# Performance work log

Hardware: AMD Instinct MI355X
Metric: run time of the kernel (lower is better)

The kernel has to match this reference:

```python
import jax, jax.numpy as jnp
import numpy as np

BS, SL, D, H = 8, 1024, 1024, 16
DK = D // H


def setup_inputs() -> dict:
    key = jax.random.key(0)
    ks = jax.random.split(key, 12)
    mk = lambda k, shape, s=1.0: jax.random.normal(k, shape, dtype=jnp.float32) * s
    return {
        "q": mk(ks[0], (BS, SL, D)),
        "k": mk(ks[1], (BS, SL, D)),
        "v": mk(ks[2], (BS, SL, D)),
        "mask": jax.random.randint(ks[3], (BS, SL), 0, 2, dtype=jnp.int32),
        "wq": mk(ks[4], (D, D), 0.02), "bq": jnp.zeros((D,), jnp.float32),
        "wk": mk(ks[5], (D, D), 0.02), "bk": jnp.zeros((D,), jnp.float32),
        "wv": mk(ks[6], (D, D), 0.02), "bv": jnp.zeros((D,), jnp.float32),
        "wo": mk(ks[7], (D, D), 0.02), "bo": jnp.zeros((D,), jnp.float32),
    }


def reference(q, k, v, mask, wq, bq, wk, bk, wv, bv, wo, bo):
    bs, sl, d = q.shape
    # linear projections (torch Linear: x @ W^T + b), split heads -> [b, h, s, dk]
    def proj(x, w, b):
        return (x @ w.T + b).reshape(bs, sl, H, DK).transpose(0, 2, 1, 3)
    qh, kh, vh = proj(q, wq, bq), proj(k, wk, bk), proj(v, wv, bv)
    # scaled scores [b, h, sq, sk]
    scores = jnp.einsum("bhqd,bhkd->bhqk", qh, kh) / jnp.sqrt(jnp.float32(DK))
    # mask query rows: mask [b, s] -> [b, 1, s, 1]
    m = mask[:, None, :, None]
    scores = jnp.where(m == 0, jnp.float32(-1e9), scores)
    # NOTE: original code computes transform(scores) but discards it; the output
    # path uses the raw masked/scaled scores (dropout is identity at eval).
    ctx = jnp.einsum("bhqk,bhkd->bhqd", scores, vh)  # [b, h, s, dk]
    concat = ctx.transpose(0, 2, 1, 3).reshape(bs, sl, d)
    return concat @ wo.T + bo
```

## Files before the change

### kernel.cpp

```cpp
#include <hip/hip_runtime.h>
#include <hip/hip_bf16.h>
#include <stdint.h>

#define BSZ 8
#define SLEN 1024
#define DMODEL 1024
#define NH 16
#define HD 64
#define MROWS (BSZ * SLEN)

typedef __bf16 bf16_t;
typedef __bf16 bf16x8 __attribute__((ext_vector_type(8)));
typedef __bf16 bf16x4 __attribute__((ext_vector_type(4)));
typedef float f32x4 __attribute__((ext_vector_type(4)));

__device__ __forceinline__ void gload_lds16(const void* g, void* l) {
    __builtin_amdgcn_global_load_lds(
        (const __attribute__((address_space(1))) unsigned int*)g,
        (__attribute__((address_space(3))) unsigned int*)l,
        16, 0, 0);
}

__global__ __launch_bounds__(256) void cvt_f32_to_bf16(
    const float* __restrict__ src, bf16_t* __restrict__ dst, int n4) {
    int i = blockIdx.x * blockDim.x + threadIdx.x;
    if (i >= n4) return;
    const float4 v = reinterpret_cast<const float4*>(src)[i];
    bf16x4 o;
    o[0] = (bf16_t)v.x; o[1] = (bf16_t)v.y; o[2] = (bf16_t)v.z; o[3] = (bf16_t)v.w;
    reinterpret_cast<bf16x4*>(dst)[i] = o;
}

template <int FINAL>
__global__ __launch_bounds__(256) void gemm_bt(
    const bf16_t* __restrict__ A, const bf16_t* __restrict__ B,
    void* __restrict__ C, const float* __restrict__ bias,
    const float* __restrict__ trow, const int* __restrict__ mask,
    int M, int N, int K, int bstride) {
    __shared__ bf16_t As[128 * 32];
    __shared__ bf16_t Bs[128 * 32];
    const int tid = threadIdx.x;
    const int m0 = blockIdx.y * 128;
    const int n0 = blockIdx.x * 128;
    const bf16_t* Bp = B + (size_t)(m0 >> 10) * (size_t)bstride;

    const int srow = tid >> 2;
    const int scol = (tid & 3) * 8;
    const bf16_t* Ag = A + (size_t)(m0 + srow) * K + scol;
    const bf16_t* Bg = Bp + (size_t)(n0 + srow) * K + scol;
    bf16_t* Asl = As + srow * 32 + scol;
    bf16_t* Bsl = Bs + srow * 32 + scol;

    const int lane = tid & 63;
    const int wave = tid >> 6;
    const int wr = (wave >> 1) * 64;
    const int wc = (wave & 1) * 64;
    const int lr = lane & 15;
    const int lk = (lane >> 4) * 8;

    f32x4 acc[4][4] = {};

    for (int kt = 0; kt < K; kt += 32) {
        gload_lds16(Ag + kt, Asl);
        gload_lds16(Ag + kt + (size_t)64 * K, Asl + 64 * 32);
        gload_lds16(Bg + kt, Bsl);
        gload_lds16(Bg + kt + (size_t)64 * K, Bsl + 64 * 32);
        __syncthreads();
        bf16x8 aw[4], bw[4];
#pragma unroll
        for (int i = 0; i < 4; ++i)
            aw[i] = *reinterpret_cast<const bf16x8*>(&As[(wr + i * 16 + lr) * 32 + lk]);
#pragma unroll
        for (int i = 0; i < 4; ++i)
            bw[i] = *reinterpret_cast<const bf16x8*>(&Bs[(wc + i * 16 + lr) * 32 + lk]);
#pragma unroll
        for (int mi = 0; mi < 4; ++mi)
#pragma unroll
            for (int ni = 0; ni < 4; ++ni)
                acc[mi][ni] = __builtin_amdgcn_mfma_f32_16x16x32_bf16(
                    aw[mi], bw[ni], acc[mi][ni], 0, 0, 0);
        __syncthreads();
    }

    const int lq4 = (lane >> 4) * 4;
    if (FINAL == 0) {
        bf16_t* Co = (bf16_t*)C;
#pragma unroll
        for (int mi = 0; mi < 4; ++mi)
#pragma unroll
            for (int ni = 0; ni < 4; ++ni) {
                const int col = n0 + wc + ni * 16 + lr;
                const float bcol = bias[col];
#pragma unroll
                for (int r = 0; r < 4; ++r) {
                    const int row = m0 + wr + mi * 16 + lq4 + r;
                    Co[(size_t)row * N + col] = (bf16_t)(acc[mi][ni][r] + bcol);
                }
            }
    } else {
        float* Co = (float*)C;
#pragma unroll
        for (int mi = 0; mi < 4; ++mi)
#pragma unroll
            for (int ni = 0; ni < 4; ++ni) {
                const int col = n0 + wc + ni * 16 + lr;
                const float bcol = bias[col];
#pragma unroll
                for (int r = 0; r < 4; ++r) {
                    const int row = m0 + wr + mi * 16 + lq4 + r;
                    const int b = row >> 10, s = row & 1023;
                    float v;
                    if (mask[b * SLEN + s]) v = acc[mi][ni][r] * 0.125f + bcol;
                    else v = trow[(size_t)b * DMODEL + col];
                    Co[(size_t)row * N + col] = v;
                }
            }
    }
}

__global__ __launch_bounds__(512) void compute_w(
    const bf16_t* __restrict__ Kh, const bf16_t* __restrict__ Vh,
    float* __restrict__ Wpart) {
    __shared__ float Ksf[64 * 64];
    __shared__ float Vsf[64 * 64];
    const int h = blockIdx.x;
    const int b = blockIdx.y;
    const int ks = blockIdx.z;
    const int tid = threadIdx.x;
    const int dd = tid & 63;
    const int eg = tid >> 6;
    const int srow = tid >> 3;
    const int sseg = (tid & 7) * 8;

    float acc[8] = {};
    for (int kc = 0; kc < 8; ++kc) {
        const int kbase = ks * 512 + kc * 64;
        const size_t roff = (size_t)(b * SLEN + kbase + srow) * DMODEL + h * HD + sseg;
        bf16x8 kv = *reinterpret_cast<const bf16x8*>(&Kh[roff]);
        bf16x8 vv = *reinterpret_cast<const bf16x8*>(&Vh[roff]);
#pragma unroll
        for (int j = 0; j < 8; ++j) {
            Ksf[srow * 64 + sseg + j] = (float)kv[j];
            Vsf[srow * 64 + sseg + j] = (float)vv[j];
        }
        __syncthreads();
#pragma unroll 4
        for (int kk = 0; kk < 64; ++kk) {
            const float vval = Vsf[kk * 64 + dd];
#pragma unroll
            for (int i = 0; i < 8; ++i)
                acc[i] += Ksf[kk * 64 + eg * 8 + i] * vval;
        }
        __syncthreads();
    }
    float* Wo = Wpart + (((size_t)ks * BSZ + b) * NH + h) * 4096;
#pragma unroll
    for (int i = 0; i < 8; ++i)
        Wo[(eg * 8 + i) * 64 + dd] = acc[i];
}

__global__ __launch_bounds__(256) void colsum_v(
    const bf16_t* __restrict__ Vh, float* __restrict__ Spart) {
    const int dseg = blockIdx.x;
    const int b = blockIdx.y;
    const int ks = blockIdx.z;
    const int d = dseg * 256 + threadIdx.x;
    float acc = 0.f;
#pragma unroll 8
    for (int k = ks * 128; k < ks * 128 + 128; ++k)
        acc += (float)Vh[(size_t)(b * SLEN + k) * DMODEL + d];
    Spart[((size_t)ks * BSZ + b) * DMODEL + d] = acc;
}

__global__ __launch_bounds__(256) void compute_t(
    const float* __restrict__ Spart, const float* __restrict__ wo,
    const float* __restrict__ bo, float* __restrict__ t) {
    __shared__ float Ss[DMODEL];
    const int b = blockIdx.x >> 8;
    const int j0 = (blockIdx.x & 255) * 4;
    const int tid = threadIdx.x;
#pragma unroll
    for (int i = 0; i < 4; ++i) {
        const int d = i * 256 + tid;
        float s = 0.f;
#pragma unroll
        for (int ks = 0; ks < 8; ++ks) s += Spart[((size_t)ks * BSZ + b) * DMODEL + d];
        Ss[d] = s;
    }
    __syncthreads();
    const int wave = tid >> 6, lane = tid & 63;
    const int j = j0 + wave;
    f32x4 acc = {};
#pragma unroll
    for (int it = 0; it < 4; ++it) {
        const int idx = it * 256 + lane * 4;
        const f32x4 wv = *reinterpret_cast<const f32x4*>(&wo[(size_t)j * DMODEL + idx]);
        const f32x4 sv = *reinterpret_cast<const f32x4*>(&Ss[idx]);
        acc += wv * sv;
    }
    float tot = acc[0] + acc[1] + acc[2] + acc[3];
#pragma unroll
    for (int off = 1; off < 64; off <<= 1) tot += __shfl_xor(tot, off, 64);
    if (lane == 0) t[(size_t)b * DMODEL + j] = -1e9f * tot + bo[j];
}

__global__ __launch_bounds__(256) void compute_pt(
    const float* __restrict__ Wpart, const float* __restrict__ wo,
    bf16_t* __restrict__ PT) {
    __shared__ float Ws[64 * 65];
    __shared__ float Wos[128 * 64];
    const int jt = blockIdx.x;
    const int h = blockIdx.y;
    const int b = blockIdx.z;
    const int tid = threadIdx.x;
    const int j0 = jt * 128;
    const float* W0 = Wpart + (((size_t)0 * BSZ + b) * NH + h) * 4096;
    const float* W1 = Wpart + (((size_t)1 * BSZ + b) * NH + h) * 4096;
#pragma unroll
    for (int i = 0; i < 16; ++i) {
        const int idx = i * 256 + tid;
        Ws[(idx >> 6) * 65 + (idx & 63)] = W0[idx] + W1[idx];
    }
#pragma unroll
    for (int i = 0; i < 32; ++i) {
        const int idx = i * 256 + tid;
        Wos[idx] = wo[(size_t)(j0 + (idx >> 6)) * DMODEL + h * HD + (idx & 63)];
    }
    __syncthreads();
    const int e = tid & 63;
    const int jb = tid >> 6;
    for (int jj2 = 0; jj2 < 32; ++jj2) {
        const int jj = jb * 32 + jj2;
        float acc = 0.f;
#pragma unroll
        for (int dd = 0; dd < 64; ++dd)
            acc += Wos[jj * 64 + dd] * Ws[e * 65 + dd];
        PT[((size_t)b * SLEN + j0 + jj) * DMODEL + h * HD + e] = (bf16_t)acc;
    }
}

extern "C" void kernel_launch(void* const* d_in, const int* in_sizes, int n_in,
                              void* d_out, int out_size, void* d_ws, size_t ws_size,
                              hipStream_t stream) {
    const float* q  = (const float*)d_in[0];
    const float* k  = (const float*)d_in[1];
    const float* v  = (const float*)d_in[2];
    const int* mask = (const int*)d_in[3];
    const float* wq = (const float*)d_in[4];
    const float* bq = (const float*)d_in[5];
    const float* wk = (const float*)d_in[6];
    const float* bk = (const float*)d_in[7];
    const float* wv = (const float*)d_in[8];
    const float* bv = (const float*)d_in[9];
    const float* wo = (const float*)d_in[10];
    const float* bo = (const float*)d_in[11];

    char* ws = (char*)d_ws;
    const size_t SZ_ACT = (size_t)MROWS * DMODEL * 2;
    const size_t SZ_W = (size_t)DMODEL * DMODEL * 2;
    bf16_t* buf0 = (bf16_t*)(ws);
    bf16_t* buf1 = (bf16_t*)(ws + SZ_ACT);
    bf16_t* buf2 = (bf16_t*)(ws + 2 * SZ_ACT);
    bf16_t* Qh   = (bf16_t*)(ws + 3 * SZ_ACT);
    bf16_t* wqb  = (bf16_t*)(ws + 4 * SZ_ACT);
    bf16_t* wkb  = (bf16_t*)(ws + 4 * SZ_ACT + SZ_W);
    bf16_t* wvb  = (bf16_t*)(ws + 4 * SZ_ACT + 2 * SZ_W);
    float* Wpart = (float*)(ws + 4 * SZ_ACT + 3 * SZ_W);
    float* Spart = (float*)((char*)Wpart + (size_t)2 * 8 * 16 * 4096 * 4);
    float* trow  = (float*)((char*)Spart + (size_t)8 * 8 * 1024 * 4);

    const int n4a = MROWS * DMODEL / 4;
    const int n4w = DMODEL * DMODEL / 4;
    cvt_f32_to_bf16<<<dim3(n4a / 256), 256, 0, stream>>>(q, buf0, n4a);
    cvt_f32_to_bf16<<<dim3(n4a / 256), 256, 0, stream>>>(k, buf1, n4a);
    cvt_f32_to_bf16<<<dim3(n4a / 256), 256, 0, stream>>>(v, buf2, n4a);
    cvt_f32_to_bf16<<<dim3(n4w / 256), 256, 0, stream>>>(wq, wqb, n4w);
    cvt_f32_to_bf16<<<dim3(n4w / 256), 256, 0, stream>>>(wk, wkb, n4w);
    cvt_f32_to_bf16<<<dim3(n4w / 256), 256, 0, stream>>>(wv, wvb, n4w);

    const dim3 gg(DMODEL / 128, MROWS / 128);
    gemm_bt<0><<<gg, 256, 0, stream>>>(buf0, wqb, Qh,   bq, nullptr, nullptr, MROWS, DMODEL, DMODEL, 0);
    gemm_bt<0><<<gg, 256, 0, stream>>>(buf1, wkb, buf0, bk, nullptr, nullptr, MROWS, DMODEL, DMODEL, 0);
    gemm_bt<0><<<gg, 256, 0, stream>>>(buf2, wvb, buf1, bv, nullptr, nullptr, MROWS, DMODEL, DMODEL, 0);

    compute_w<<<dim3(NH, BSZ, 2), 512, 0, stream>>>(buf0, buf1, Wpart);
    colsum_v<<<dim3(4, BSZ, 8), 256, 0, stream>>>(buf1, Spart);
    compute_t<<<dim3(2048), 256, 0, stream>>>(Spart, wo, bo, trow);
    compute_pt<<<dim3(8, NH, BSZ), 256, 0, stream>>>(Wpart, wo, buf2);

    gemm_bt<1><<<gg, 256, 0, stream>>>(Qh, buf2, d_out, bo, trow, mask,
                                       MROWS, DMODEL, DMODEL, SLEN * DMODEL);
}
```

Before: 384.2 us.

## Replace 128x128 GEMM with double-buffered 256x256 swizzled-LDS kernel and batch launches

Replaces the 128x128 single-buffered bf16 GEMM with a 256x256-tile, 512-thread kernel. It double-buffers LDS, prefetches the next K slice with direct global-to-LDS loads while issuing MFMAs, uses an XOR-style swizzle to cut LDS bank conflicts, and raises wave priority around MFMA bursts. The QKV projections are batched into one launch over blockIdx.z when workspace allows, and the six conversion kernels are merged into two. The aim is more data reuse per tile, hidden load latency and less launch overhead. The cost is larger LDS use, which limits occupancy, and a bigger workspace footprint on the roomy path.

```diff
diff --git a/kernel.cpp b/kernel.cpp
--- a/kernel.cpp
+++ b/kernel.cpp
@@ -8,6 +8,7 @@
 #define NH 16
 #define HD 64
 #define MROWS (BSZ * SLEN)
+#define NT 16
 
 typedef __bf16 bf16_t;
 typedef __bf16 bf16x8 __attribute__((ext_vector_type(8)));
@@ -17,102 +18,168 @@
 __device__ __forceinline__ void gload_lds16(const void* g, void* l) {
     __builtin_amdgcn_global_load_lds(
         (const __attribute__((address_space(1))) unsigned int*)g,
-        (__attribute__((address_space(3))) unsigned int*)l,
-        16, 0, 0);
-}
-
-__global__ __launch_bounds__(256) void cvt_f32_to_bf16(
-    const float* __restrict__ src, bf16_t* __restrict__ dst, int n4) {
+        (__attribute__((address_space(3))) unsigned int*)l, 16, 0, 0);
+}
+
+__global__ __launch_bounds__(256) void cvt3(
+    const float* __restrict__ s0, const float* __restrict__ s1, const float* __restrict__ s2,
+    bf16_t* __restrict__ o0, bf16_t* __restrict__ o1, bf16_t* __restrict__ o2, int n4) {
+    const float* s = s0; bf16_t* d = o0;
+    if (blockIdx.y == 1) { s = s1; d = o1; }
+    else if (blockIdx.y == 2) { s = s2; d = o2; }
     int i = blockIdx.x * blockDim.x + threadIdx.x;
     if (i >= n4) return;
-    const float4 v = reinterpret_cast<const float4*>(src)[i];
+    const float4 v = reinterpret_cast<const float4*>(s)[i];
     bf16x4 o;
     o[0] = (bf16_t)v.x; o[1] = (bf16_t)v.y; o[2] = (bf16_t)v.z; o[3] = (bf16_t)v.w;
-    reinterpret_cast<bf16x4*>(dst)[i] = o;
+    reinterpret_cast<bf16x4*>(d)[i] = o;
+}
+
+__device__ __forceinline__ void mfma_quad(f32x4 (&acc)[8][4], int mb,
+                                          const bf16x8 (&afr)[4], const bf16x8 (&bfr)[4]) {
+    __builtin_amdgcn_s_setprio(1);
+#pragma unroll
+    for (int m = 0; m < 4; ++m)
+#pragma unroll
+        for (int n = 0; n < 4; ++n)
+            acc[mb + m][n] = __builtin_amdgcn_mfma_f32_16x16x32_bf16(
+                afr[m], bfr[n], acc[mb + m][n], 0, 0, 0);
+    __builtin_amdgcn_s_setprio(0);
 }
 
 template <int FINAL>
-__global__ __launch_bounds__(256) void gemm_bt(
-    const bf16_t* __restrict__ A, const bf16_t* __restrict__ B,
-    void* __restrict__ C, const float* __restrict__ bias,
-    const float* __restrict__ trow, const int* __restrict__ mask,
-    int M, int N, int K, int bstride) {
-    __shared__ bf16_t As[128 * 32];
-    __shared__ bf16_t Bs[128 * 32];
+__global__ __launch_bounds__(512, 2) void gemm256(
+    const bf16_t* __restrict__ A0, const bf16_t* __restrict__ B0p, void* __restrict__ C0, const float* __restrict__ bias0,
+    const bf16_t* __restrict__ A1, const bf16_t* __restrict__ B1p, void* __restrict__ C1, const float* __restrict__ bias1,
+    const bf16_t* __restrict__ A2, const bf16_t* __restrict__ B2p, void* __restrict__ C2, const float* __restrict__ bias2,
+    const float* __restrict__ trow, const int* __restrict__ mask) {
+    __shared__ __align__(16) bf16_t As[4][256 * 32];
+    __shared__ __align__(16) bf16_t Bs[4][256 * 32];
     const int tid = threadIdx.x;
-    const int m0 = blockIdx.y * 128;
-    const int n0 = blockIdx.x * 128;
-    const bf16_t* Bp = B + (size_t)(m0 >> 10) * (size_t)bstride;
-
-    const int srow = tid >> 2;
-    const int scol = (tid & 3) * 8;
-    const bf16_t* Ag = A + (size_t)(m0 + srow) * K + scol;
-    const bf16_t* Bg = Bp + (size_t)(n0 + srow) * K + scol;
-    bf16_t* Asl = As + srow * 32 + scol;
-    bf16_t* Bsl = Bs + srow * 32 + scol;
-
-    const int lane = tid & 63;
-    const int wave = tid >> 6;
-    const int wr = (wave >> 1) * 64;
-    const int wc = (wave & 1) * 64;
-    const int lr = lane & 15;
-    const int lk = (lane >> 4) * 8;
-
-    f32x4 acc[4][4] = {};
-
-    for (int kt = 0; kt < K; kt += 32) {
-        gload_lds16(Ag + kt, Asl);
-        gload_lds16(Ag + kt + (size_t)64 * K, Asl + 64 * 32);
-        gload_lds16(Bg + kt, Bsl);
-        gload_lds16(Bg + kt + (size_t)64 * K, Bsl + 64 * 32);
-        __syncthreads();
-        bf16x8 aw[4], bw[4];
-#pragma unroll
-        for (int i = 0; i < 4; ++i)
-            aw[i] = *reinterpret_cast<const bf16x8*>(&As[(wr + i * 16 + lr) * 32 + lk]);
-#pragma unroll
-        for (int i = 0; i < 4; ++i)
-            bw[i] = *reinterpret_cast<const bf16x8*>(&Bs[(wc + i * 16 + lr) * 32 + lk]);
-#pragma unroll
-        for (int mi = 0; mi < 4; ++mi)
-#pragma unroll
-            for (int ni = 0; ni < 4; ++ni)
-                acc[mi][ni] = __builtin_amdgcn_mfma_f32_16x16x32_bf16(
-                    aw[mi], bw[ni], acc[mi][ni], 0, 0, 0);
-        __syncthreads();
-    }
-
-    const int lq4 = (lane >> 4) * 4;
+    const int lane = tid & 63, wave = tid >> 6;
+    const int wm = wave >> 2, wn = wave & 3;
+    const int lr = lane & 15, g = lane >> 4;
+
+    const bf16_t* A = A0; const bf16_t* B = B0p; void* C = C0; const float* bias = bias0;
+    if (blockIdx.z == 1) { A = A1; B = B1p; C = C1; bias = bias1; }
+    else if (blockIdx.z == 2) { A = A2; B = B2p; C = C2; bias = bias2; }
+
+    const int m0 = blockIdx.y * 256;
+    const int n0 = blockIdx.x * 256;
+    if (FINAL) B += (size_t)(m0 >> 10) * SLEN * DMODEL;
+
+    const int q0 = wave * 64 + lane, q1 = 512 + q0;
+    const int row0 = q0 >> 2, row1 = q1 >> 2;
+    const int gl0 = ((q0 & 3) - (row0 >> 1)) & 3;
+    const int gl1 = ((q1 & 3) - (row1 >> 1)) & 3;
+    const int sOfs0 = row0 * DMODEL + gl0 * 8;
+    const int sOfs1 = row1 * DMODEL + gl1 * 8;
+    const bf16_t* Ag = A + (size_t)m0 * DMODEL;
+    const bf16_t* Bg = B + (size_t)n0 * DMODEL;
+    char* const AsB = (char*)&As[0][0];
+    char* const BsB = (char*)&Bs[0][0];
+    const int d0 = q0 * 16, d1 = q1 * 16;
+
+    int aoff[8], boff[4];
+#pragma unroll
+    for (int mi = 0; mi < 8; ++mi) {
+        const int r = wm * 128 + mi * 16 + lr;
+        aoff[mi] = r * 64 + (((g + (r >> 1)) & 3) << 4);
+    }
+#pragma unroll
+    for (int ni = 0; ni < 4; ++ni) {
+        const int r = wn * 64 + ni * 16 + lr;
+        boff[ni] = r * 64 + (((g + (r >> 1)) & 3) << 4);
+    }
+
+    f32x4 acc[8][4] = {};
+
+    gload_lds16(Ag + sOfs0, AsB + d0);
+    gload_lds16(Ag + sOfs1, AsB + d1);
+    gload_lds16(Bg + sOfs0, BsB + d0);
+    gload_lds16(Bg + sOfs1, BsB + d1);
+    gload_lds16(Ag + sOfs0 + 32, AsB + 16384 + d0);
+    gload_lds16(Ag + sOfs1 + 32, AsB + 16384 + d1);
+    gload_lds16(Bg + sOfs0 + 32, BsB + 16384 + d0);
+    gload_lds16(Bg + sOfs1 + 32, BsB + 16384 + d1);
+
+    for (int t = 0; t < NT; ++t) {
+        const int cur = t & 1, nxt = cur ^ 1;
+        const int kn = ((t + 1 < NT) ? (t + 1) : 0) * 64;
+        const char* Ac0 = AsB + cur * 32768;
+        const char* Ac1 = Ac0 + 16384;
+        const char* Bc0 = BsB + cur * 32768;
+        const char* Bc1 = Bc0 + 16384;
+        char* An0 = AsB + nxt * 32768; char* An1 = An0 + 16384;
+        char* Bn0 = BsB + nxt * 32768; char* Bn1 = Bn0 + 16384;
+        bf16x8 afr[4], bfr[4];
+
+        asm volatile("s_waitcnt vmcnt(4)" ::: "memory");
+        __builtin_amdgcn_s_barrier();
+        __builtin_amdgcn_sched_barrier(0);
+        gload_lds16(Ag + sOfs0 + kn, An0 + d0);
+        gload_lds16(Ag + sOfs1 + kn, An0 + d1);
+#pragma unroll
+        for (int i = 0; i < 4; ++i) bfr[i] = *reinterpret_cast<const bf16x8*>(Bc0 + boff[i]);
+#pragma unroll
+        for (int i = 0; i < 4; ++i) afr[i] = *reinterpret_cast<const bf16x8*>(Ac0 + aoff[i]);
+        mfma_quad(acc, 0, afr, bfr);
+
+        gload_lds16(Bg + sOfs0 + kn, Bn0 + d0);
+        gload_lds16(Bg + sOfs1 + kn, Bn0 + d1);
+#pragma unroll
+        for (int i = 0; i < 4; ++i) afr[i] = *reinterpret_cast<const bf16x8*>(Ac0 + aoff[4 + i]);
+        mfma_quad(acc, 4, afr, bfr);
+
+        asm volatile("s_waitcnt vmcnt(4)" ::: "memory");
+        __builtin_amdgcn_s_barrier();
+        __builtin_amdgcn_sched_barrier(0);
+        gload_lds16(Ag + sOfs0 + kn + 32, An1 + d0);
+        gload_lds16(Ag + sOfs1 + kn + 32, An1 + d1);
+#pragma unroll
+        for (int i = 0; i < 4; ++i) bfr[i] = *reinterpret_cast<const bf16x8*>(Bc1 + boff[i]);
+#pragma unroll
+        for (int i = 0; i < 4; ++i) afr[i] = *reinterpret_cast<const bf16x8*>(Ac1 + aoff[i]);
+        mfma_quad(acc, 0, afr, bfr);
+
+        gload_lds16(Bg + sOfs0 + kn + 32, Bn1 + d0);
+        gload_lds16(Bg + sOfs1 + kn + 32, Bn1 + d1);
+#pragma unroll
+        for (int i = 0; i < 4; ++i) afr[i] = *reinterpret_cast<const bf16x8*>(Ac1 + aoff[4 + i]);
+        mfma_quad(acc, 4, afr, bfr);
+    }
+
+    const int lq4 = g * 4;
     if (FINAL == 0) {
         bf16_t* Co = (bf16_t*)C;
 #pragma unroll
-        for (int mi = 0; mi < 4; ++mi)
+        for (int mi = 0; mi < 8; ++mi)
 #pragma unroll
             for (int ni = 0; ni < 4; ++ni) {
-                const int col = n0 + wc + ni * 16 + lr;
+                const int col = n0 + wn * 64 + ni * 16 + lr;
                 const float bcol = bias[col];
 #pragma unroll
                 for (int r = 0; r < 4; ++r) {
-                    const int row = m0 + wr + mi * 16 + lq4 + r;
-                    Co[(size_t)row * N + col] = (bf16_t)(acc[mi][ni][r] + bcol);
+                    const int row = m0 + wm * 128 + mi * 16 + lq4 + r;
+                    Co[(size_t)row * DMODEL + col] = (bf16_t)(acc[mi][ni][r] + bcol);
                 }
             }
     } else {
         float* Co = (float*)C;
 #pragma unroll
-        for (int mi = 0; mi < 4; ++mi)
+        for (int mi = 0; mi < 8; ++mi)
 #pragma unroll
             for (int ni = 0; ni < 4; ++ni) {
-                const int col = n0 + wc + ni * 16 + lr;
+                const int col = n0 + wn * 64 + ni * 16 + lr;
                 const float bcol = bias[col];
 #pragma unroll
                 for (int r = 0; r < 4; ++r) {
-                    const int row = m0 + wr + mi * 16 + lq4 + r;
+                    const int row = m0 + wm * 128 + mi * 16 + lq4 + r;
                     const int b = row >> 10, s = row & 1023;
                     float v;
                     if (mask[b * SLEN + s]) v = acc[mi][ni][r] * 0.125f + bcol;
                     else v = trow[(size_t)b * DMODEL + col];
-                    Co[(size_t)row * N + col] = v;
+                    Co[(size_t)row * DMODEL + col] = v;
                 }
             }
     }
@@ -258,36 +325,56 @@
     char* ws = (char*)d_ws;
     const size_t SZ_ACT = (size_t)MROWS * DMODEL * 2;
     const size_t SZ_W = (size_t)DMODEL * DMODEL * 2;
-    bf16_t* buf0 = (bf16_t*)(ws);
-    bf16_t* buf1 = (bf16_t*)(ws + SZ_ACT);
-    bf16_t* buf2 = (bf16_t*)(ws + 2 * SZ_ACT);
-    bf16_t* Qh   = (bf16_t*)(ws + 3 * SZ_ACT);
-    bf16_t* wqb  = (bf16_t*)(ws + 4 * SZ_ACT);
-    bf16_t* wkb  = (bf16_t*)(ws + 4 * SZ_ACT + SZ_W);
-    bf16_t* wvb  = (bf16_t*)(ws + 4 * SZ_ACT + 2 * SZ_W);
-    float* Wpart = (float*)(ws + 4 * SZ_ACT + 3 * SZ_W);
-    float* Spart = (float*)((char*)Wpart + (size_t)2 * 8 * 16 * 4096 * 4);
-    float* trow  = (float*)((char*)Spart + (size_t)8 * 8 * 1024 * 4);
+    const size_t SZ_WPART = (size_t)2 * 8 * 16 * 4096 * 4;
+    const size_t SZ_SPART = (size_t)8 * 8 * 1024 * 4;
+    const size_t SZ_TROW = (size_t)8 * 1024 * 4;
+    const size_t need_roomy = 6 * SZ_ACT + 3 * SZ_W + SZ_WPART + SZ_SPART + SZ_TROW;
+    const bool roomy = ws_size >= need_roomy;
+
+    bf16_t* qb = (bf16_t*)(ws);
+    bf16_t* kb = (bf16_t*)(ws + SZ_ACT);
+    bf16_t* vb = (bf16_t*)(ws + 2 * SZ_ACT);
+    bf16_t* Qh = (bf16_t*)(ws + 3 * SZ_ACT);
+    bf16_t *Kh, *Vh, *PT;
+    char* tail;
+    if (roomy) {
+        Kh = (bf16_t*)(ws + 4 * SZ_ACT);
+        Vh = (bf16_t*)(ws + 5 * SZ_ACT);
+        PT = qb;
+        tail = ws + 6 * SZ_ACT;
+    } else {
+        Kh = qb; Vh = kb; PT = vb;
+        tail = ws + 4 * SZ_ACT;
+    }
+    bf16_t* wqb = (bf16_t*)(tail);
+    bf16_t* wkb = (bf16_t*)(tail + SZ_W);
+    bf16_t* wvb = (bf16_t*)(tail + 2 * SZ_W);
+    float* Wpart = (float*)(tail + 3 * SZ_W);
+    float* Spart = (float*)(tail + 3 * SZ_W + SZ_WPART);
+    float* trow  = (float*)(tail + 3 * SZ_W + SZ_WPART + SZ_SPART);
 
     const int n4a = MROWS * DMODEL / 4;
     const int n4w = DMODEL * DMODEL / 4;
-    cvt_f32_to_bf16<<<dim3(n4a / 256), 256, 0, stream>>>(q, buf0, n4a);
-    cvt_f32_to_bf16<<<dim3(n4a / 256), 256, 0, stream>>>(k, buf1, n4a);
-    cvt_f32_to_bf16<<<dim3(n4a / 256), 256, 0, stream>>>(v, buf2, n4a);
-    cvt_f32_to_bf16<<<dim3(n4w / 256), 256, 0, stream>>>(wq, wqb, n4w);
-    cvt_f32_to_bf16<<<dim3(n4w / 256), 256, 0, stream>>>(wk, wkb, n4w);
-    cvt_f32_to_bf16<<<dim3(n4w / 256), 256, 0, stream>>>(wv, wvb, n4w);
-
-    const dim3 gg(DMODEL / 128, MROWS / 128);
-    gemm_bt<0><<<gg, 256, 0, stream>>>(buf0, wqb, Qh,   bq, nullptr, nullptr, MROWS, DMODEL, DMODEL, 0);
-    gemm_bt<0><<<gg, 256, 0, stream>>>(buf1, wkb, buf0, bk, nullptr, nullptr, MROWS, DMODEL, DMODEL, 0);
-    gemm_bt<0><<<gg, 256, 0, stream>>>(buf2, wvb, buf1, bv, nullptr, nullptr, MROWS, DMODEL, DMODEL, 0);
-
-    compute_w<<<dim3(NH, BSZ, 2), 512, 0, stream>>>(buf0, buf1, Wpart);
-    colsum_v<<<dim3(4, BSZ, 8), 256, 0, stream>>>(buf1, Spart);
+    cvt3<<<dim3(n4a / 256, 3), 256, 0, stream>>>(q, k, v, qb, kb, vb, n4a);
+    cvt3<<<dim3(n4w / 256, 3), 256, 0, stream>>>(wq, wk, wv, wqb, wkb, wvb, n4w);
+
+    if (roomy) {
+        gemm256<0><<<dim3(4, 32, 3), 512, 0, stream>>>(
+            qb, wqb, Qh, bq, kb, wkb, Kh, bk, vb, wvb, Vh, bv, nullptr, nullptr);
+    } else {
+        gemm256<0><<<dim3(4, 32, 1), 512, 0, stream>>>(
+            qb, wqb, Qh, bq, qb, wqb, Qh, bq, qb, wqb, Qh, bq, nullptr, nullptr);
+        gemm256<0><<<dim3(4, 32, 1), 512, 0, stream>>>(
+            kb, wkb, Kh, bk, kb, wkb, Kh, bk, kb, wkb, Kh, bk, nullptr, nullptr);
+        gemm256<0><<<dim3(4, 32, 1), 512, 0, stream>>>(
+            vb, wvb, Vh, bv, vb, wvb, Vh, bv, vb, wvb, Vh, bv, nullptr, nullptr);
+    }
+
+    compute_w<<<dim3(NH, BSZ, 2), 512, 0, stream>>>(Kh, Vh, Wpart);
+    colsum_v<<<dim3(4, BSZ, 8), 256, 0, stream>>>(Vh, Spart);
     compute_t<<<dim3(2048), 256, 0, stream>>>(Spart, wo, bo, trow);
-    compute_pt<<<dim3(8, NH, BSZ), 256, 0, stream>>>(Wpart, wo, buf2);
-
-    gemm_bt<1><<<gg, 256, 0, stream>>>(Qh, buf2, d_out, bo, trow, mask,
-                                       MROWS, DMODEL, DMODEL, SLEN * DMODEL);
-}
+    compute_pt<<<dim3(8, NH, BSZ), 256, 0, stream>>>(Wpart, wo, PT);
+
+    gemm256<1><<<dim3(4, 32, 1), 512, 0, stream>>>(
+        Qh, PT, d_out, bo, Qh, PT, d_out, bo, Qh, PT, d_out, bo, trow, mask);
+}
```

New measurement: 350.9 us. -8.7%, faster.
